# Performance work log

Measured on AMD Instinct MI355X. Metric: run time of the kernel, lower is better.

The kernel has to match this reference:

```python
import jax, jax.numpy as jnp
import numpy as np

B, S, D, H = 4, 1024, 1024, 16
DH = D // H
K_SPARSE = 32
LAMBDA_MAX, ALPHA = 10.0, 5.0
SPARSE_THRESHOLD = 1.0


def setup_inputs() -> dict:
    key = jax.random.key(0)
    ks = jax.random.split(key, 12)
    x = jax.random.normal(ks[0], (B, S, D), dtype=jnp.float32)
    prior_mask = jax.random.bernoulli(ks[1], 0.1, (S, S))
    prior_indices = jax.random.randint(ks[2], (S, K_SPARSE), 0, S)
    prior_index_mask = jax.random.bernoulli(ks[3], 0.9, (S, K_SPARSE))
    prior_index_mask = prior_index_mask.at[:, 0].set(True)  # avoid all-masked rows
    u_prev = jax.random.normal(ks[4], (B, 1), dtype=jnp.float32)
    sc = 1.0 / np.sqrt(D)
    Wq = jax.random.normal(ks[5], (D, D), dtype=jnp.float32) * sc
    Wk = jax.random.normal(ks[6], (D, D), dtype=jnp.float32) * sc
    Wv = jax.random.normal(ks[7], (D, D), dtype=jnp.float32) * sc
    Wo = jax.random.normal(ks[8], (D, D), dtype=jnp.float32) * sc
    bq = jnp.zeros((D,), jnp.float32)
    bk = jnp.zeros((D,), jnp.float32)
    bv = jnp.zeros((D,), jnp.float32)
    bo = jnp.zeros((D,), jnp.float32)
    return {"x": x, "prior_mask": prior_mask, "prior_indices": prior_indices,
            "prior_index_mask": prior_index_mask, "u_prev": u_prev,
            "Wq": Wq, "bq": bq, "Wk": Wk, "bk": bk, "Wv": Wv, "bv": bv,
            "Wo": Wo, "bo": bo}


def reference(x, prior_mask, prior_indices, prior_index_mask, u_prev,
              Wq, bq, Wk, bk, Wv, bv, Wo, bo):
    Bb, Ss, Dd = x.shape
    scale = 1.0 / jnp.sqrt(jnp.asarray(DH, x.dtype))

    def proj(W, b):
        return (x @ W.T + b).reshape(Bb, Ss, H, DH).transpose(0, 2, 1, 3)  # [B,H,S,DH]

    Q, K, V = proj(Wq, bq), proj(Wk, bk), proj(Wv, bv)

    lam = LAMBDA_MAX * jnp.exp(-ALPHA * u_prev.reshape(Bb))  # [B]
    use_sparse = lam >= SPARSE_THRESHOLD                      # [B] bool

    # ---- dense branch: full SDPA with lambda-scaled prior bias ----
    scores = jnp.einsum('bhqd,bhkd->bhqk', Q, K) * scale      # [B,H,S,S]
    prior_bias = jnp.where(prior_mask[:Ss, :Ss], 0.0, -1.0).astype(x.dtype)
    bias = lam[:, None, None, None] * prior_bias[None, None]
    dense_out = jnp.einsum('bhqk,bhkd->bhqd',
                           jax.nn.softmax(scores + bias, axis=-1), V)

    # ---- sparse branch: gather-indexed SDPA over prior_indices ----
    idx = prior_indices[:Ss]                                   # [S,k]
    Kg = K[:, :, idx]                                          # [B,H,S,k,DH]
    Vg = V[:, :, idx]
    s_scores = jnp.einsum('bhsd,bhskd->bhsk', Q, Kg) * scale   # [B,H,S,k]
    s_scores = jnp.where(prior_index_mask[:Ss][None, None], s_scores,
                         jnp.asarray(-jnp.inf, x.dtype))
    sparse_out = jnp.einsum('bhsk,bhskd->bhsd',
                            jax.nn.softmax(s_scores, axis=-1), Vg)

    out = jnp.where(use_sparse[:, None, None, None], sparse_out, dense_out)
    out = out.transpose(0, 2, 1, 3).reshape(Bb, Ss, Dd)
    return out @ Wo.T + bo
```

## Files before the change

### kernel.cpp

```cpp
#include <hip/hip_runtime.h>
#include <hip/hip_bf16.h>
#include <cmath>

#define NB 4
#define NS 1024
#define ND 1024
#define NH 16
#define NDH 64
#define NKSP 32
#define SCALE 0.125f
#define LOG2E 1.44269504f
#define SCALE2 (SCALE * LOG2E)

typedef __attribute__((ext_vector_type(8))) short bf16x8;
typedef __attribute__((ext_vector_type(4))) float f32x4;
typedef unsigned long long u64;

#define AS1 __attribute__((address_space(1)))
#define AS3 __attribute__((address_space(3)))

__device__ __forceinline__ void gl_lds16(const void* g, void* l) {
    __builtin_amdgcn_global_load_lds((const AS1 void*)g, (AS3 void*)l, 16, 0, 0);
}

__device__ __forceinline__ ushort f2bf(float f) {
    union { __hip_bfloat16 h; ushort u; } cv;
    cv.h = __float2bfloat16(f);
    return cv.u;
}
__device__ __forceinline__ float bf2f(ushort u) {
    union { unsigned int i; float f; } cv;
    cv.i = ((unsigned int)u) << 16;
    return cv.f;
}
__device__ __forceinline__ float fexp2(float x) {
    return __builtin_amdgcn_exp2f(x);
}

__global__ __launch_bounds__(256)
void f2bf_multi(const float* __restrict__ x,
                const float* __restrict__ w0, const float* __restrict__ w1,
                const float* __restrict__ w2, const float* __restrict__ w3,
                const int* __restrict__ pm,
                ushort* __restrict__ xo,
                ushort* __restrict__ o0, ushort* __restrict__ o1,
                ushort* __restrict__ o2, ushort* __restrict__ o3,
                u64* __restrict__ bm)
{
    int y = blockIdx.y;
    if (y == 5) {
        int word = blockIdx.x * 4 + (threadIdx.x >> 6);
        int lane = threadIdx.x & 63;
        int row  = word >> 4, wcol = word & 15;
        int v = pm[(size_t)row * NS + wcol * 64 + lane];
        u64 b = __ballot(v != 0);
        if (lane == 0) bm[word] = b;
        return;
    }
    const float* src; ushort* dst; int nblk;
    if (y == 0)      { src = x;  dst = xo; nblk = 4096; }
    else if (y == 1) { src = w0; dst = o0; nblk = 1024; }
    else if (y == 2) { src = w1; dst = o1; nblk = 1024; }
    else if (y == 3) { src = w2; dst = o2; nblk = 1024; }
    else             { src = w3; dst = o3; nblk = 1024; }
    if (blockIdx.x >= (unsigned)nblk) return;
    int i = (blockIdx.x * 256 + threadIdx.x) * 4;
    float4 v = *(const float4*)&src[i];
    ushort4 o;
    o.x = f2bf(v.x); o.y = f2bf(v.y); o.z = f2bf(v.z); o.w = f2bf(v.w);
    *(ushort4*)&dst[i] = o;
}

__global__ __launch_bounds__(256)
void gemm_qkv(const ushort* __restrict__ xb,
              const ushort* __restrict__ Wqb, const ushort* __restrict__ Wkb,
              const ushort* __restrict__ Wvb,
              const float* __restrict__ bq, const float* __restrict__ bk,
              const float* __restrict__ bv,
              ushort* __restrict__ Qo, ushort* __restrict__ Ko,
              ushort* __restrict__ Vo, ushort* __restrict__ Vto)
{
    constexpr int K = ND;
    __shared__ __attribute__((aligned(16))) ushort As[128 * 32];
    __shared__ __attribute__((aligned(16))) ushort Bs[128 * 32];

    const int tid  = threadIdx.x;
    const int lane = tid & 63, w = tid >> 6;
    const int wm = w >> 1, wn = w & 1;
    const int which = blockIdx.x >> 3;
    const int n0 = (blockIdx.x & 7) * 128;
    const int m0 = blockIdx.y * 128;
    const int quad = lane >> 4, l16 = lane & 15;

    const ushort* W = (which == 0) ? Wqb : (which == 1) ? Wkb : Wvb;
    const float* bias = (which == 0) ? bq : (which == 1) ? bk : bv;
    ushort* Out = (which == 0) ? Qo : (which == 1) ? Ko : Vo;

    f32x4 acc[4][4] = {};

    for (int k0 = 0; k0 < K; k0 += 32) {
        __syncthreads();
#pragma unroll
        for (int u = 0; u < 2; ++u) {
            int t0 = u * 256 + w * 64;
            int t  = t0 + lane;
            int row = t >> 2, kc = (t & 3) * 8;
            gl_lds16(xb + (size_t)(m0 + row) * K + k0 + kc, &As[t0 * 8]);
            gl_lds16(W  + (size_t)(n0 + row) * K + k0 + kc, &Bs[t0 * 8]);
        }
        __syncthreads();

        bf16x8 af[4], bfr[4];
#pragma unroll
        for (int mt = 0; mt < 4; ++mt)
            af[mt] = *(const bf16x8*)&As[(wm*64 + mt*16 + l16) * 32 + quad*8];
#pragma unroll
        for (int nt = 0; nt < 4; ++nt)
            bfr[nt] = *(const bf16x8*)&Bs[(wn*64 + nt*16 + l16) * 32 + quad*8];
#pragma unroll
        for (int mt = 0; mt < 4; ++mt)
#pragma unroll
            for (int nt = 0; nt < 4; ++nt)
                acc[mt][nt] = __builtin_amdgcn_mfma_f32_16x16x32_bf16(
                    af[mt], bfr[nt], acc[mt][nt], 0, 0, 0);
    }

#pragma unroll
    for (int nt = 0; nt < 4; ++nt) {
        int n = n0 + wn*64 + nt*16 + l16;
        float bz = bias[n];
        int hh = n >> 6, dh = n & 63;
#pragma unroll
        for (int mt = 0; mt < 4; ++mt) {
#pragma unroll
            for (int rg = 0; rg < 4; ++rg) {
                int m = m0 + wm*64 + mt*16 + quad*4 + rg;
                int b = m >> 10, s = m & (NS - 1);
                ushort val = f2bf(acc[mt][nt][rg] + bz);
                Out[(((size_t)(b*NH + hh))*NS + s)*NDH + dh] = val;
                if (which == 2)
                    Vto[(((size_t)(b*NH + hh))*NDH + dh)*NS + s] = val;
            }
        }
    }
}

__global__ __launch_bounds__(256)
void gemm_out(const ushort* __restrict__ A, const ushort* __restrict__ W,
              const float* __restrict__ bias, float* __restrict__ Cout)
{
    constexpr int K = ND;
    __shared__ __attribute__((aligned(16))) ushort As[64 * 32];
    __shared__ __attribute__((aligned(16))) ushort Bs[128 * 32];

    const int tid  = threadIdx.x;
    const int lane = tid & 63, w = tid >> 6;
    const int wm = w & 1, wn = w >> 1;
    const int m0 = blockIdx.y * 64, n0 = blockIdx.x * 128;
    const int quad = lane >> 4, l16 = lane & 15;

    f32x4 acc[2][4] = {};

    for (int k0 = 0; k0 < K; k0 += 32) {
        __syncthreads();
        {
            int t0 = w * 64;
            int t  = t0 + lane;
            int row = t >> 2, kc = (t & 3) * 8;
            gl_lds16(A + (size_t)(m0 + row) * K + k0 + kc, &As[t0 * 8]);
        }
#pragma unroll
        for (int u = 0; u < 2; ++u) {
            int t0 = u * 256 + w * 64;
            int t  = t0 + lane;
            int row = t >> 2, kc = (t & 3) * 8;
            gl_lds16(W + (size_t)(n0 + row) * K + k0 + kc, &Bs[t0 * 8]);
        }
        __syncthreads();

        bf16x8 af[2], bfr[4];
#pragma unroll
        for (int mt = 0; mt < 2; ++mt)
            af[mt] = *(const bf16x8*)&As[(wm*32 + mt*16 + l16) * 32 + quad*8];
#pragma unroll
        for (int nt = 0; nt < 4; ++nt)
            bfr[nt] = *(const bf16x8*)&Bs[(wn*64 + nt*16 + l16) * 32 + quad*8];
#pragma unroll
        for (int mt = 0; mt < 2; ++mt)
#pragma unroll
            for (int nt = 0; nt < 4; ++nt)
                acc[mt][nt] = __builtin_amdgcn_mfma_f32_16x16x32_bf16(
                    af[mt], bfr[nt], acc[mt][nt], 0, 0, 0);
    }

#pragma unroll
    for (int nt = 0; nt < 4; ++nt) {
        int n = n0 + wn*64 + nt*16 + l16;
        float bz = bias[n];
#pragma unroll
        for (int mt = 0; mt < 2; ++mt) {
#pragma unroll
            for (int rg = 0; rg < 4; ++rg) {
                int m = m0 + wm*32 + mt*16 + quad*4 + rg;
                Cout[(size_t)m * ND + n] = acc[mt][nt][rg] + bz;
            }
        }
    }
}

#define LOADK(DST, KT)                                                        \
    _Pragma("unroll")                                                         \
    for (int nt = 0; nt < 4; ++nt)                                            \
        _Pragma("unroll")                                                     \
        for (int kk = 0; kk < 2; ++kk)                                        \
            DST[nt][kk] = *(const bf16x8*)                                    \
                &Kh[(size_t)((KT)*64 + nt*16 + l16) * NDH + kk*32 + quad*8];

#define LOADV(DST, KT)                                                        \
    _Pragma("unroll")                                                         \
    for (int nt = 0; nt < 4; ++nt)                                            \
        _Pragma("unroll")                                                     \
        for (int kk = 0; kk < 2; ++kk)                                        \
            DST[nt][kk] = *(const bf16x8*)                                    \
                &Vth[(size_t)(nt*16 + l16) * NS + (KT)*64 + kk*32 + quad*8];

#define STEP(KT, KF, VF)                                                      \
    _Pragma("unroll")                                                         \
    for (int qh = 0; qh < 2; ++qh) {                                          \
        const int qrow = w*32 + qh*16 + l16;                                  \
        u64 wq = MW[(KT)*128 + qrow] >> (quad * 4);                           \
        f32x4 s_acc[4] = {};                                                  \
        __builtin_amdgcn_s_setprio(1);                                        \
        _Pragma("unroll")                                                     \
        for (int nt = 0; nt < 4; ++nt)                                        \
            _Pragma("unroll")                                                 \
            for (int kk = 0; kk < 2; ++kk)                                    \
                s_acc[nt] = __builtin_amdgcn_mfma_f32_16x16x32_bf16(          \
                    KF[nt][kk], qf[qh][kk], s_acc[nt], 0, 0, 0);              \
        __builtin_amdgcn_s_setprio(0);                                        \
        _Pragma("unroll")                                                     \
        for (int nt = 0; nt < 4; ++nt) {                                      \
            ushort4 pk;                                                       \
            float p0 = fexp2(fmaf(s_acc[nt][0], SCALE2,                       \
                 ((wq >> (nt*16 + 0)) & 1ULL) ? 0.f : nlam2));                \
            float p1 = fexp2(fmaf(s_acc[nt][1], SCALE2,                       \
                 ((wq >> (nt*16 + 1)) & 1ULL) ? 0.f : nlam2));                \
            float p2 = fexp2(fmaf(s_acc[nt][2], SCALE2,                       \
                 ((wq >> (nt*16 + 2)) & 1ULL) ? 0.f : nlam2));                \
            float p3 = fexp2(fmaf(s_acc[nt][3], SCALE2,                       \
                 ((wq >> (nt*16 + 3)) & 1ULL) ? 0.f : nlam2));                \
            pk.x = f2bf(p0); pk.y = f2bf(p1);                                 \
            pk.z = f2bf(p2); pk.w = f2bf(p3);                                 \
            *(ushort4*)&Ps[qrow*72 + nt*16 + quad*4] = pk;                    \
        }                                                                     \
        bf16x8 pf[2];                                                         \
        _Pragma("unroll")                                                     \
        for (int kk = 0; kk < 2; ++kk)                                        \
            pf[kk] = *(const bf16x8*)&Ps[qrow*72 + kk*32 + quad*8];           \
        __builtin_amdgcn_s_setprio(1);                                        \
        _Pragma("unroll")                                                     \
        for (int kk = 0; kk < 2; ++kk) {                                      \
            l_acc[qh] = __builtin_amdgcn_mfma_f32_16x16x32_bf16(              \
                pf[kk], ones.v, l_acc[qh], 0, 0, 0);                          \
            _Pragma("unroll")                                                 \
            for (int nt = 0; nt < 4; ++nt)                                    \
                o_acc[qh][nt] = __builtin_amdgcn_mfma_f32_16x16x32_bf16(      \
                    pf[kk], VF[nt][kk], o_acc[qh][nt], 0, 0, 0);              \
        }                                                                     \
        __builtin_amdgcn_s_setprio(0);                                        \
    }

__global__ __launch_bounds__(256, 2)
void attn_kernel(const ushort* __restrict__ Qb, const ushort* __restrict__ Kb,
                 const ushort* __restrict__ Vb, const ushort* __restrict__ Vt,
                 const u64* __restrict__ bm,
                 const int* __restrict__ pidx, const int* __restrict__ pimask,
                 const float* __restrict__ u_prev, ushort* __restrict__ OA)
{
    __shared__ __attribute__((aligned(16))) ushort Ps[128 * 72];
    __shared__ __attribute__((aligned(16))) u64    MW[16 * 128];

    const int tid  = threadIdx.x;
    const int lane = tid & 63, w = tid >> 6;
    const int quad = lane >> 4, l16 = lane & 15;

    const int id    = blockIdx.x;
    const int xcd   = id & 7;
    const int t5    = id >> 3;
    const int qtile = t5 & 7;
    const int head  = (t5 >> 3) * 8 + xcd;
    const int b = head >> 4, h = head & 15;
    const int s0 = qtile * 128;

    const float lam = 10.0f * __expf(-5.0f * u_prev[b]);
    const bool sparse = (lam >= 1.0f);

    const size_t bh = (size_t)b * NH + h;
    const ushort* Qh  = Qb + bh * NS * NDH;
    const ushort* Kh  = Kb + bh * NS * NDH;
    const ushort* Vh  = Vb + bh * NS * NDH;
    const ushort* Vth = Vt + bh * NDH * NS;

    if (!sparse) {
        const float nlam2 = -lam * LOG2E;

#pragma unroll
        for (int u = 0; u < 8; ++u) {
            int idx = u * 256 + tid;
            int row = idx >> 4, wd = idx & 15;
            MW[wd * 128 + row] = bm[(size_t)s0 * 16 + idx];
        }
        __syncthreads();

        bf16x8 qf[2][2];
#pragma unroll
        for (int qh = 0; qh < 2; ++qh)
#pragma unroll
            for (int kk = 0; kk < 2; ++kk)
                qf[qh][kk] = *(const bf16x8*)
                    &Qh[(size_t)(s0 + w*32 + qh*16 + l16) * NDH + kk*32 + quad*8];

        union { bf16x8 v; ushort s[8]; } ones;
#pragma unroll
        for (int i = 0; i < 8; ++i) ones.s[i] = 0x3F80;

        f32x4 o_acc[2][4] = {};
        f32x4 l_acc[2] = {};

        bf16x8 kfA[4][2], vfA[4][2], kfB[4][2], vfB[4][2];
        LOADK(kfA, 0);
        LOADV(vfA, 0);

        for (int kt = 0; kt < 16; kt += 2) {
            LOADK(kfB, kt + 1);
            LOADV(vfB, kt + 1);
            STEP(kt, kfA, vfA);

            if (kt + 2 < 16) {
                LOADK(kfA, kt + 2);
                LOADV(vfA, kt + 2);
            }
            STEP(kt + 1, kfB, vfB);
        }

#pragma unroll
        for (int qh = 0; qh < 2; ++qh) {
            float inv[4];
#pragma unroll
            for (int rg = 0; rg < 4; ++rg) inv[rg] = 1.f / l_acc[qh][rg];
#pragma unroll
            for (int nt = 0; nt < 4; ++nt)
#pragma unroll
                for (int rg = 0; rg < 4; ++rg) {
                    int m = w*32 + qh*16 + quad*4 + rg;
                    OA[((size_t)b*NS + s0 + m)*ND + h*NDH + nt*16 + l16] =
                        f2bf(o_acc[qh][nt][rg] * inv[rg]);
                }
        }
    } else {
        const int r2  = lane & 15;
        const int cg  = lane >> 4;
#pragma unroll
        for (int qh = 0; qh < 2; ++qh) {
            const int row = w*32 + qh*16 + r2;

            float qreg[64];
            {
                const ushort* qp = Qh + (size_t)(s0 + row) * NDH;
#pragma unroll
                for (int c = 0; c < 8; ++c) {
                    union { bf16x8 v; ushort s[8]; } qv;
                    qv.v = *(const bf16x8*)(qp + c*8);
#pragma unroll
                    for (int j = 0; j < 8; ++j) qreg[c*8 + j] = bf2f(qv.s[j]);
                }
            }

            float sc[8];
#pragma unroll
            for (int jj = 0; jj < 8; ++jj) {
                int j  = cg*8 + jj;
                int mv = pimask[(size_t)(s0+row)*NKSP + j];
                if (mv) {
                    int kv = pidx[(size_t)(s0+row)*NKSP + j];
                    const ushort* krow = &Kh[(size_t)kv * NDH];
                    float acc = 0.f;
#pragma unroll
                    for (int c = 0; c < 8; ++c) {
                        union { bf16x8 v; ushort s[8]; } kk;
                        kk.v = *(const bf16x8*)(krow + c*8);
#pragma unroll
                        for (int jb = 0; jb < 8; ++jb)
                            acc = fmaf(qreg[c*8 + jb], bf2f(kk.s[jb]), acc);
                    }
                    sc[jj] = acc * SCALE;
                } else {
                    sc[jj] = -INFINITY;
                }
            }
            float mt = sc[0];
#pragma unroll
            for (int jj = 1; jj < 8; ++jj) mt = fmaxf(mt, sc[jj]);
            mt = fmaxf(mt, __shfl_xor(mt, 16));
            mt = fmaxf(mt, __shfl_xor(mt, 32));

            float psum = 0.f;
#pragma unroll
            for (int jj = 0; jj < 8; ++jj) {
                float p = __expf(sc[jj] - mt);
                psum += p;
                Ps[row * 72 + cg*8 + jj] = f2bf(p);
            }
            psum += __shfl_xor(psum, 16);
            psum += __shfl_xor(psum, 32);

            float o[16];
#pragma unroll
            for (int i = 0; i < 16; ++i) o[i] = 0.f;

            for (int j = 0; j < 32; ++j) {
                float p = bf2f(Ps[row * 72 + j]);
                if (p != 0.f) {
                    int kv = pidx[(size_t)(s0+row)*NKSP + j];
                    const ushort* vrow = &Vh[(size_t)kv * NDH + cg*16];
#pragma unroll
                    for (int c = 0; c < 2; ++c) {
                        union { bf16x8 v; ushort s[8]; } vv;
                        vv.v = *(const bf16x8*)(vrow + c*8);
#pragma unroll
                        for (int jb = 0; jb < 8; ++jb)
                            o[c*8 + jb] = fmaf(p, bf2f(vv.s[jb]), o[c*8 + jb]);
                    }
                }
            }

            float inv = 1.f / psum;
            ushort* op = OA + ((size_t)b*NS + s0 + row)*ND + h*NDH + cg*16;
#pragma unroll
            for (int i4 = 0; i4 < 4; ++i4) {
                ushort4 v;
                v.x = f2bf(o[i4*4+0]*inv); v.y = f2bf(o[i4*4+1]*inv);
                v.z = f2bf(o[i4*4+2]*inv); v.w = f2bf(o[i4*4+3]*inv);
                *(ushort4*)(op + i4*4) = v;
            }
        }
    }
}

extern "C" void kernel_launch(void* const* d_in, const int* in_sizes, int n_in,
                              void* d_out, int out_size, void* d_ws, size_t ws_size,
                              hipStream_t stream)
{
    const float* x      = (const float*)d_in[0];
    const int*   pmask  = (const int*)  d_in[1];
    const int*   pidx   = (const int*)  d_in[2];
    const int*   pimask = (const int*)  d_in[3];
    const float* u_prev = (const float*)d_in[4];
    const float* Wq     = (const float*)d_in[5];
    const float* bq     = (const float*)d_in[6];
    const float* Wk     = (const float*)d_in[7];
    const float* bk     = (const float*)d_in[8];
    const float* Wv     = (const float*)d_in[9];
    const float* bv     = (const float*)d_in[10];
    const float* Wo     = (const float*)d_in[11];
    const float* bo     = (const float*)d_in[12];
    float* out = (float*)d_out;

    const size_t QSZ = (size_t)NB * NH * NS * NDH;
    const size_t WSZ = (size_t)ND * ND;
    ushort* xb  = (ushort*)d_ws;
    ushort* Qw  = xb  + QSZ;
    ushort* Kw  = Qw  + QSZ;
    ushort* Vw  = Kw  + QSZ;
    ushort* Vtw = Vw  + QSZ;
    ushort* Awb = Vtw + QSZ;
    ushort* Wqb = Awb + QSZ;
    ushort* Wkb = Wqb + WSZ;
    ushort* Wvb = Wkb + WSZ;
    ushort* Wob = Wvb + WSZ;
    u64*    bmw = (u64*)(Wob + WSZ);

    f2bf_multi<<<dim3(4096, 6), 256, 0, stream>>>(
        x, Wq, Wk, Wv, Wo, pmask, xb, Wqb, Wkb, Wvb, Wob, bmw);

    gemm_qkv<<<dim3(24, 32), 256, 0, stream>>>(
        xb, Wqb, Wkb, Wvb, bq, bk, bv, Qw, Kw, Vw, Vtw);

    attn_kernel<<<512, 256, 0, stream>>>(
        Qw, Kw, Vw, Vtw, bmw, pidx, pimask, u_prev, Awb);

    gemm_out<<<dim3(ND/128, (NB*NS)/64), 256, 0, stream>>>(Awb, Wob, bo, out);
}
```

Measured before the change: 237.0 us.

## Stage dense-branch K/V tiles cooperatively into swizzled double-buffered LDS

Before this change, each of the four waves in the dense attention branch loaded the full K and V tiles from global memory into registers itself, so the same data was fetched four times per block. Now the block copies each 64-key K/V tile once into LDS with async global-to-LDS loads. An XOR swizzle avoids bank conflicts, and two buffers let the next tile load while the current one is computed. Each wave then reads its fragments from LDS. This adds 32KB of shared memory per block and a barrier every iteration, which may limit occupancy and reduce latency hiding.

```diff
diff --git a/kernel.cpp b/kernel.cpp
--- a/kernel.cpp
+++ b/kernel.cpp
@@ -208,21 +208,36 @@
     }
 }
 
-#define LOADK(DST, KT)                                                        \
+
+#define STAGE(BUF, KT)                                                        \
+    _Pragma("unroll")                                                         \
+    for (int u = 0; u < 4; ++u) {                                             \
+        int cb = w * 256 + u * 64;                                            \
+        int c  = cb + lane;                                                   \
+        const ushort* src;                                                    \
+        if (w < 2) {                                                          \
+            int row = c >> 3, sub = c & 7;                                    \
+            src = Kh + (((size_t)((KT)*64 + row)) << 6)                       \
+                     + ((sub ^ (row & 7)) << 3);                              \
+        } else {                                                              \
+            int c2 = c - 512;                                                 \
+            int row = c2 >> 3, sub = c2 & 7;                                  \
+            src = Vth + (size_t)row * NS + (KT)*64                            \
+                      + ((sub ^ (row & 7)) << 3);                             \
+        }                                                                     \
+        gl_lds16(src, (ushort*)&KV[BUF][0][0] + (size_t)cb * 8);              \
+    }
+
+#define LOADKV(KF, VF, BUF)                                                   \
     _Pragma("unroll")                                                         \
     for (int nt = 0; nt < 4; ++nt)                                            \
         _Pragma("unroll")                                                     \
-        for (int kk = 0; kk < 2; ++kk)                                        \
-            DST[nt][kk] = *(const bf16x8*)                                    \
-                &Kh[(size_t)((KT)*64 + nt*16 + l16) * NDH + kk*32 + quad*8];
-
-#define LOADV(DST, KT)                                                        \
-    _Pragma("unroll")                                                         \
-    for (int nt = 0; nt < 4; ++nt)                                            \
-        _Pragma("unroll")                                                     \
-        for (int kk = 0; kk < 2; ++kk)                                        \
-            DST[nt][kk] = *(const bf16x8*)                                    \
-                &Vth[(size_t)(nt*16 + l16) * NS + (KT)*64 + kk*32 + quad*8];
+        for (int kk = 0; kk < 2; ++kk) {                                      \
+            int rowk = nt*16 + l16;                                           \
+            int ck = (kk*4 + quad) ^ (l16 & 7);                               \
+            KF[nt][kk] = *(const bf16x8*)&KV[BUF][0][rowk*64 + ck*8];         \
+            VF[nt][kk] = *(const bf16x8*)&KV[BUF][1][rowk*64 + ck*8];         \
+        }
 
 #define STEP(KT, KF, VF)                                                      \
     _Pragma("unroll")                                                         \
@@ -279,6 +294,7 @@
 {
     __shared__ __attribute__((aligned(16))) ushort Ps[128 * 72];
     __shared__ __attribute__((aligned(16))) u64    MW[16 * 128];
+    __shared__ __attribute__((aligned(16))) ushort KV[2][2][64 * 64];
 
     const int tid  = threadIdx.x;
     const int lane = tid & 63, w = tid >> 6;
@@ -304,13 +320,13 @@
     if (!sparse) {
         const float nlam2 = -lam * LOG2E;
 
+        STAGE(0, 0);
 #pragma unroll
         for (int u = 0; u < 8; ++u) {
             int idx = u * 256 + tid;
             int row = idx >> 4, wd = idx & 15;
             MW[wd * 128 + row] = bm[(size_t)s0 * 16 + idx];
         }
-        __syncthreads();
 
         bf16x8 qf[2][2];
 #pragma unroll
@@ -327,20 +343,16 @@
         f32x4 o_acc[2][4] = {};
         f32x4 l_acc[2] = {};
 
-        bf16x8 kfA[4][2], vfA[4][2], kfB[4][2], vfB[4][2];
-        LOADK(kfA, 0);
-        LOADV(vfA, 0);
-
-        for (int kt = 0; kt < 16; kt += 2) {
-            LOADK(kfB, kt + 1);
-            LOADV(vfB, kt + 1);
-            STEP(kt, kfA, vfA);
-
-            if (kt + 2 < 16) {
-                LOADK(kfA, kt + 2);
-                LOADV(vfA, kt + 2);
-            }
-            STEP(kt + 1, kfB, vfB);
+        __syncthreads();
+
+        int cur = 0;
+        for (int kt = 0; kt < 16; ++kt) {
+            if (kt + 1 < 16) STAGE(cur ^ 1, kt + 1);
+            bf16x8 kf[4][2], vf[4][2];
+            LOADKV(kf, vf, cur);
+            STEP(kt, kf, vf);
+            __syncthreads();
+            cur ^= 1;
         }
 
 #pragma unroll
```

New measurement: 236.4 us. Within noise of the previous version (-0.2%).
